# Kernel optimization log

Hardware: AMD Instinct MI355X
Metric: run time of the kernel (lower is better)

The kernel has to match this reference:

```python
import jax, jax.numpy as jnp
import numpy as np
from jax import lax

DILATION = 2
EPS = 1e-05


def _scales_and_weights(img_sz):
    m = min(img_sz)
    if m > 128:
        return [m // 16, m // 8, m // 4], [0.8, 0.1, 0.1]
    elif m > 64:
        return [m // 4, m // 2], [0.4, 0.6]
    else:
        return [m // 2], [1.0]


def _box_conv(z, ksz, stride):
    # all-ones 3D box filter, VALID padding, rhs (kernel) dilation = 2
    kern = jnp.ones((1, 1, ksz, ksz, ksz), dtype=z.dtype)
    return lax.conv_general_dilated(
        z, kern,
        window_strides=(stride, stride, stride),
        padding='VALID',
        rhs_dilation=(DILATION, DILATION, DILATION),
        dimension_numbers=('NCDHW', 'OIDHW', 'NCDHW'))


def setup_inputs() -> dict:
    key = jax.random.key(0)
    k1, k2 = jax.random.split(key)
    shape = (4, 1, 128, 128, 128)
    return {
        'input': jax.random.normal(k1, shape, dtype=jnp.float32),
        'target': jax.random.normal(k2, shape, dtype=jnp.float32),
    }


def reference(input, target):
    img_sz = input.shape[2:]
    scales, weights = _scales_and_weights(list(img_sz))
    B = input.shape[0]

    input_2 = input ** 2
    target_2 = target ** 2
    input_target = input * target

    lncc_total = jnp.asarray(0.0, dtype=input.dtype)
    for ksz, w in zip(scales, weights):
        step = max((ksz + 1) // 2, 1)
        conv = lambda z: _box_conv(z, ksz, step).reshape(B, -1)
        x_sum = conv(input)
        y_sum = conv(target)
        x2_sum = conv(input_2)
        y2_sum = conv(target_2)
        xy_sum = conv(input_target)

        numel = float(ksz ** 3)
        x_mean = x_sum / numel
        y_mean = y_sum / numel
        cross = xy_sum - y_mean * x_sum - x_mean * y_sum + y_mean * x_mean * numel
        x_var = x2_sum - 2 * x_mean * x_sum + x_mean ** 2 * numel
        y_var = y2_sum - 2 * y_mean * y_sum + y_mean ** 2 * numel
        lncc = cross * cross / (x_var * y_var + EPS)
        lncc_total = lncc_total + (1.0 - lncc.mean()) * w
    return lncc_total
```

## Files before the change

kernel.cpp:

```cpp
#include <hip/hip_runtime.h>


#define NSTAT 5

__global__ __launch_bounds__(512) void lncc_pass1(
    const float* __restrict__ x, const float* __restrict__ y,
    float* __restrict__ ws ) {
  const int blk = blockIdx.x;
  const int b  = blk >> 6;
  const int ci = (blk >> 3) & 7;
  const int cj = blk & 7;
  const int tid = threadIdx.x;
  const int w4 = tid & 31;
  const int r  = tid >> 5;
  const int s  = r & 7;
  const int ih = r >> 3;

  const size_t base = (size_t)b * (128 * 128 * 128)
      + (size_t)((16 * ci + 8 * ih) * (128 * 128))
      + (size_t)((16 * cj + 2 * s) * 128)
      + (size_t)(w4 * 4);

  float4 ax[4], ay[4];
#pragma unroll
  for (int i = 0; i < 4; ++i)
    ax[i] = *(const float4*)(x + base + (size_t)(i * 2 * 128 * 128));
#pragma unroll
  for (int i = 0; i < 4; ++i)
    ay[i] = *(const float4*)(y + base + (size_t)(i * 2 * 128 * 128));

  float v[NSTAT] = {0.f, 0.f, 0.f, 0.f, 0.f};
#pragma unroll
  for (int i = 0; i < 4; ++i) {
    const float xa = ax[i].x, xb = ax[i].z;
    const float ya = ay[i].x, yb = ay[i].z;
    v[0] += xa + xb;
    v[1] += ya + yb;
    v[2] += xa * xa + xb * xb;
    v[3] += ya * ya + yb * yb;
    v[4] += xa * ya + xb * yb;
  }

#pragma unroll
  for (int k = 0; k < NSTAT; ++k) {
    v[k] += __shfl_xor(v[k], 1);
    v[k] += __shfl_xor(v[k], 2);
    v[k] += __shfl_xor(v[k], 32);
  }

  const int lane = tid & 63, wave = tid >> 6, ck = w4 >> 2;
  __shared__ float sd[8 * 8 * NSTAT];
  if ((lane & 3) == 0 && lane < 32) {
#pragma unroll
    for (int k = 0; k < NSTAT; ++k) sd[(wave * 8 + ck) * NSTAT + k] = v[k];
  }
  __syncthreads();

  if (tid < 8 * NSTAT) {
    const int c2 = tid / NSTAT, k = tid % NSTAT;
    float acc = 0.f;
#pragma unroll
    for (int wv = 0; wv < 8; ++wv) acc += sd[(wv * 8 + c2) * NSTAT + k];
    ws[((b * 512) + ci * 64 + cj * 8 + c2) * NSTAT + k] = acc;
  }
}

__global__ __launch_bounds__(512) void lncc_pass2(
    const float* __restrict__ ws, float* __restrict__ out) {
  const int tid = threadIdx.x;
  __shared__ float s5[2048 * NSTAT];
  for (int i = tid; i < 2048 * NSTAT / 4; i += 512)
    ((float4*)s5)[i] = ((const float4*)ws)[i];
  __syncthreads();

  const int wave = tid >> 6, lane = tid & 63;

  __shared__ float totl[4 * NSTAT];
  if (wave < 4) {
    float tot[NSTAT] = {0.f, 0.f, 0.f, 0.f, 0.f};
    for (int c = lane; c < 512; c += 64) {
      const int idx = (wave * 512 + c) * NSTAT;
#pragma unroll
      for (int k = 0; k < NSTAT; ++k) tot[k] += s5[idx + k];
    }
#pragma unroll
    for (int off = 32; off; off >>= 1)
#pragma unroll
      for (int k = 0; k < NSTAT; ++k) tot[k] += __shfl_down(tot[k], off);
    if (lane == 0)
#pragma unroll
      for (int k = 0; k < NSTAT; ++k) totl[wave * NSTAT + k] = tot[k];
  }
  __syncthreads();

  float lsum = 0.f;
  if (tid < 500) {
    const int b2 = tid / 125, rem = tid % 125;
    const int od = rem / 25, oh = (rem / 5) % 5, ow = rem % 5;
    float a0 = 0.f, a1 = 0.f, a2 = 0.f, a3 = 0.f, a4 = 0.f;
    for (int i = od; i < od + 4; ++i)
      for (int j = oh; j < oh + 4; ++j)
        for (int k2 = ow; k2 < ow + 4; ++k2) {
          const int idx = ((b2 * 512) + i * 64 + j * 8 + k2) * NSTAT;
          a0 += s5[idx];     a1 += s5[idx + 1];
          a2 += s5[idx + 2]; a3 += s5[idx + 3];
          a4 += s5[idx + 4];
        }
    const float numel = 32768.f;
    const float cross = a4 - a0 * a1 / numel;
    const float xv    = a2 - a0 * a0 / numel;
    const float yv    = a3 - a1 * a1 / numel;
    lsum = cross * cross / (xv * yv + 1e-5f);
  }
#pragma unroll
  for (int off = 32; off; off >>= 1) lsum += __shfl_down(lsum, off);
  __shared__ float wred[8];
  if (lane == 0) wred[wave] = lsum;
  __syncthreads();

  if (tid == 0) {
    float sum32 = 0.f;
    for (int i = 0; i < 8; ++i) sum32 += wred[i];
    const float mean32 = sum32 / 500.f;
    float sum64 = 0.f;
    for (int bb = 0; bb < 4; ++bb) {
      const float X  = totl[bb * NSTAT + 0], Y  = totl[bb * NSTAT + 1];
      const float X2 = totl[bb * NSTAT + 2], Y2 = totl[bb * NSTAT + 3];
      const float XY = totl[bb * NSTAT + 4];
      const float numel = 262144.f;
      const float cross = XY - X * Y / numel;
      const float xv    = X2 - X * X / numel;
      const float yv    = Y2 - Y * Y / numel;
      sum64 += cross * cross / (xv * yv + 1e-5f);
    }
    const float mean64 = sum64 * 0.25f;
    out[0] = (1.f - mean32) * 0.4f + (1.f - mean64) * 0.6f;
  }
}

extern "C" void kernel_launch(void* const* d_in, const int* in_sizes, int n_in,
                              void* d_out, int out_size, void* d_ws, size_t ws_size,
                              hipStream_t stream) {
  const float* x = (const float*)d_in[0];
  const float* y = (const float*)d_in[1];
  float* ws = (float*)d_ws;
  lncc_pass1<<<256, 512, 0, stream>>>(x, y, ws);
  lncc_pass2<<<1, 512, 0, stream>>>(ws, (float*)d_out);
}
```

Baseline: 98.51 us.

## Compute separable box sums: w-axis prefix in pass1, h and d axes in pass2

```diff
diff --git a/kernel.cpp b/kernel.cpp
--- a/kernel.cpp
+++ b/kernel.cpp
@@ -5,7 +5,8 @@
 
 __global__ __launch_bounds__(512) void lncc_pass1(
     const float* __restrict__ x, const float* __restrict__ y,
-    float* __restrict__ ws ) {
+    float* __restrict__ wsA ,
+    float* __restrict__ wsT ) {
   const int blk = blockIdx.x;
   const int b  = blk >> 6;
   const int ci = (blk >> 3) & 7;
@@ -50,6 +51,7 @@
 
   const int lane = tid & 63, wave = tid >> 6, ck = w4 >> 2;
   __shared__ float sd[8 * 8 * NSTAT];
+  __shared__ float c8[8][NSTAT];
   if ((lane & 3) == 0 && lane < 32) {
 #pragma unroll
     for (int k = 0; k < NSTAT; ++k) sd[(wave * 8 + ck) * NSTAT + k] = v[k];
@@ -61,35 +63,59 @@
     float acc = 0.f;
 #pragma unroll
     for (int wv = 0; wv < 8; ++wv) acc += sd[(wv * 8 + c2) * NSTAT + k];
-    ws[((b * 512) + ci * 64 + cj * 8 + c2) * NSTAT + k] = acc;
+    c8[c2][k] = acc;
+  }
+  __syncthreads();
+
+  if (tid < 25) {
+    const int ow = tid / 5, k = tid % 5;
+    wsA[blk * 25 + tid] =
+        c8[ow][k] + c8[ow + 1][k] + c8[ow + 2][k] + c8[ow + 3][k];
+  } else if (tid < 30) {
+    const int k = tid - 25;
+    float t = 0.f;
+#pragma unroll
+    for (int c = 0; c < 8; ++c) t += c8[c][k];
+    wsT[blk * 5 + k] = t;
   }
 }
 
 __global__ __launch_bounds__(512) void lncc_pass2(
-    const float* __restrict__ ws, float* __restrict__ out) {
+    const float* __restrict__ wsA, const float* __restrict__ wsT,
+    float* __restrict__ out) {
   const int tid = threadIdx.x;
-  __shared__ float s5[2048 * NSTAT];
-  for (int i = tid; i < 2048 * NSTAT / 4; i += 512)
-    ((float4*)s5)[i] = ((const float4*)ws)[i];
+  const int wave = tid >> 6, lane = tid & 63;
+  __shared__ float lA[6400];
+  __shared__ float lT[1280];
+  __shared__ float s2[4000];
+  __shared__ float totl[4 * NSTAT];
+  __shared__ float wred[8];
+
+  for (int i = tid; i < 1600; i += 512)
+    ((float4*)lA)[i] = ((const float4*)wsA)[i];
+  for (int i = tid; i < 320; i += 512)
+    ((float4*)lT)[i] = ((const float4*)wsT)[i];
   __syncthreads();
 
-  const int wave = tid >> 6, lane = tid & 63;
+  for (int e = tid; e < 4000; e += 512) {
+    const int k = e % 5, r1 = e / 5;
+    const int ow = r1 % 5, r2 = r1 / 5;
+    const int oh = r2 % 5, bc = r2 / 5;
+    const int bs = (bc * 8 + oh) * 25 + ow * 5 + k;
+    s2[e] = lA[bs] + lA[bs + 25] + lA[bs + 50] + lA[bs + 75];
+  }
 
-  __shared__ float totl[4 * NSTAT];
   if (wave < 4) {
-    float tot[NSTAT] = {0.f, 0.f, 0.f, 0.f, 0.f};
-    for (int c = lane; c < 512; c += 64) {
-      const int idx = (wave * 512 + c) * NSTAT;
+    float t[NSTAT];
 #pragma unroll
-      for (int k = 0; k < NSTAT; ++k) tot[k] += s5[idx + k];
-    }
+    for (int k = 0; k < NSTAT; ++k) t[k] = lT[(wave * 64 + lane) * 5 + k];
 #pragma unroll
     for (int off = 32; off; off >>= 1)
 #pragma unroll
-      for (int k = 0; k < NSTAT; ++k) tot[k] += __shfl_down(tot[k], off);
+      for (int k = 0; k < NSTAT; ++k) t[k] += __shfl_down(t[k], off);
     if (lane == 0)
 #pragma unroll
-      for (int k = 0; k < NSTAT; ++k) totl[wave * NSTAT + k] = tot[k];
+      for (int k = 0; k < NSTAT; ++k) totl[wave * NSTAT + k] = t[k];
   }
   __syncthreads();
 
@@ -97,24 +123,19 @@
   if (tid < 500) {
     const int b2 = tid / 125, rem = tid % 125;
     const int od = rem / 25, oh = (rem / 5) % 5, ow = rem % 5;
-    float a0 = 0.f, a1 = 0.f, a2 = 0.f, a3 = 0.f, a4 = 0.f;
-    for (int i = od; i < od + 4; ++i)
-      for (int j = oh; j < oh + 4; ++j)
-        for (int k2 = ow; k2 < ow + 4; ++k2) {
-          const int idx = ((b2 * 512) + i * 64 + j * 8 + k2) * NSTAT;
-          a0 += s5[idx];     a1 += s5[idx + 1];
-          a2 += s5[idx + 2]; a3 += s5[idx + 3];
-          a4 += s5[idx + 4];
-        }
+    const int bs = (((b2 * 8 + od) * 5 + oh) * 5 + ow) * 5;
+    float a[NSTAT];
+#pragma unroll
+    for (int k = 0; k < NSTAT; ++k)
+      a[k] = s2[bs + k] + s2[bs + 125 + k] + s2[bs + 250 + k] + s2[bs + 375 + k];
     const float numel = 32768.f;
-    const float cross = a4 - a0 * a1 / numel;
-    const float xv    = a2 - a0 * a0 / numel;
-    const float yv    = a3 - a1 * a1 / numel;
+    const float cross = a[4] - a[0] * a[1] / numel;
+    const float xv    = a[2] - a[0] * a[0] / numel;
+    const float yv    = a[3] - a[1] * a[1] / numel;
     lsum = cross * cross / (xv * yv + 1e-5f);
   }
 #pragma unroll
   for (int off = 32; off; off >>= 1) lsum += __shfl_down(lsum, off);
-  __shared__ float wred[8];
   if (lane == 0) wred[wave] = lsum;
   __syncthreads();
 
@@ -143,7 +164,8 @@
                               hipStream_t stream) {
   const float* x = (const float*)d_in[0];
   const float* y = (const float*)d_in[1];
-  float* ws = (float*)d_ws;
-  lncc_pass1<<<256, 512, 0, stream>>>(x, y, ws);
-  lncc_pass2<<<1, 512, 0, stream>>>(ws, (float*)d_out);
+  float* wsA = (float*)d_ws;
+  float* wsT = (float*)((char*)d_ws + 6400 * 4);
+  lncc_pass1<<<256, 512, 0, stream>>>(x, y, wsA, wsT);
+  lncc_pass2<<<1, 512, 0, stream>>>(wsA, wsT, (float*)d_out);
 }
```

Measured after the change: 91.97 us. 1.07x faster.
